# Kernel optimization log

Hardware: AMD Instinct MI355X
Metric: run time of the kernel (lower is better)

The kernel has to match this reference:

```python
import jax, jax.numpy as jnp
import numpy as np

B, S, H = 1, 2048, 2048
NH, KVH, D = 32, 8, 64
G = NH // KVH  # num_key_value_groups = 4


def setup_inputs() -> dict:
    key = jax.random.key(0)
    k1, k2, k3 = jax.random.split(key, 3)
    x = jax.random.normal(k1, (B, S, H), dtype=jnp.float32)
    w_qkv = jax.random.normal(k2, ((NH + 2 * KVH) * D, H), dtype=jnp.float32) * 0.02
    w_o = jax.random.normal(k3, (H, NH * D), dtype=jnp.float32) * 0.02
    return {"x": x, "w_qkv": w_qkv, "w_o": w_o}


def _rope_cos_sin(seqlen, dim, dtype):
    inv_freq = 1.0 / (10000.0 ** (jnp.arange(0, dim, 2, dtype=jnp.float32) / dim))
    t = jnp.arange(seqlen, dtype=jnp.float32)
    freqs = jnp.outer(t, inv_freq)  # [S, D/2]
    return jnp.cos(freqs).astype(dtype), jnp.sin(freqs).astype(dtype)


def _apply_rope(x, cos, sin):
    # x: [B,S,h,D]; non-interleaved half rotation (flash-attn RotaryEmbedding)
    d2 = x.shape[-1] // 2
    x1, x2 = x[..., :d2], x[..., d2:]
    c = cos[None, :, None, :]
    s = sin[None, :, None, :]
    return jnp.concatenate([x1 * c - x2 * s, x2 * c + x1 * s], axis=-1)


def reference(x, w_qkv, w_o):
    b, s, _ = x.shape
    qkv = x @ w_qkv.T  # fused QKV proj: [B,S,(NH+2*KVH)*D]
    q, kv = jnp.split(qkv, [NH * D], axis=-1)
    q = q.reshape(b, s, NH, D)
    kv = kv.reshape(b, s, 2, KVH, D)
    cos, sin = _rope_cos_sin(s, D, x.dtype)
    q = _apply_rope(q, cos, sin)
    k = _apply_rope(kv[:, :, 0], cos, sin)
    v = kv[:, :, 1]
    # GQA: group q heads per kv head instead of repeat_interleave (same math)
    qg = q.reshape(b, s, KVH, G, D)
    scale = 1.0 / np.sqrt(D).astype(np.float32)
    scores = jnp.einsum('bskgd,btkd->bkgst', qg, k) * scale  # [B,KVH,G,S,S]
    causal = jnp.tril(jnp.ones((s, s), dtype=bool))
    scores = jnp.where(causal[None, None, None], scores, jnp.asarray(-jnp.inf, scores.dtype))
    p = jax.nn.softmax(scores, axis=-1)
    out = jnp.einsum('bkgst,btkd->bskgd', p, v).reshape(b, s, NH * D)
    return out @ w_o.T
```

## Files before the change

kernel.cpp:

```cpp
#include <hip/hip_runtime.h>


typedef __bf16 bf16_t;
typedef __attribute__((ext_vector_type(8))) __bf16 bf16x8;
typedef __attribute__((ext_vector_type(4))) __bf16 bf16x4;
typedef __attribute__((ext_vector_type(4))) float f32x4;

#define S_LEN 2048
#define H_DIM 2048
#define NHEAD 32
#define KVH 8
#define HD 64
#define QKV_N 3072

#define ENT_STRIDE 8320

__global__ void cast3_kernel(const float* __restrict__ x, const float* __restrict__ wq,
                             const float* __restrict__ wo, bf16_t* __restrict__ xb,
                             bf16_t* __restrict__ wqb, bf16_t* __restrict__ wob) {
  int i = blockIdx.x * blockDim.x + threadIdx.x;
  const int n1 = S_LEN * H_DIM / 4, n2 = QKV_N * H_DIM / 4, n3 = H_DIM * H_DIM / 4;
  const float* src; bf16_t* dst; int j;
  if (i < n1)           { src = x;  dst = xb;  j = i; }
  else if (i < n1 + n2) { src = wq; dst = wqb; j = i - n1; }
  else if (i < n1 + n2 + n3) { src = wo; dst = wob; j = i - n1 - n2; }
  else return;
  float4 v = ((const float4*)src)[j];
  bf16x4 o;
  o.x = (bf16_t)v.x; o.y = (bf16_t)v.y; o.z = (bf16_t)v.z; o.w = (bf16_t)v.w;
  ((bf16x4*)dst)[j] = o;
}

__device__ __forceinline__ void async_copy16(bf16_t* lds_base, const bf16_t* g) {
  __builtin_amdgcn_global_load_lds(
      (const __attribute__((address_space(1))) unsigned int*)g,
      (__attribute__((address_space(3))) unsigned int*)lds_base, 16, 0, 0);
}

#define GBM 128
#define GBN 128

template <int EPI>
__global__ __launch_bounds__(512, 4) void gemm_sk(const bf16_t* __restrict__ A,
                                                  const bf16_t* __restrict__ B,
                                                  float* __restrict__ C,
                                                  bf16_t* __restrict__ qb,
                                                  bf16_t* __restrict__ ktp,
                                                  bf16_t* __restrict__ vt2,
                                                  int M, int N, int K) {
  __shared__ __align__(16) bf16_t As[2][GBM * 64];
  __shared__ __align__(16) bf16_t Bs[2][GBM * 64];

  const int tid  = threadIdx.x;
  const int lane = tid & 63;
  const int w    = tid >> 6;
  const int wq   = w & 3;
  const int gw   = w >> 2;
  const int wm   = (wq >> 1) * 64;
  const int wn   = (wq & 1) * 64;
  const int c    = lane & 15;
  const int quad = lane >> 4;
  const int m0   = blockIdx.y * GBM;
  const int n0   = blockIdx.x * GBN;

  f32x4 acc[4][4] = {};

  const bf16_t* Ab = A + (size_t)m0 * K;
  const bf16_t* Bb = B + (size_t)n0 * K;

  int srow[2], skc[2], sb[2];
#pragma unroll
  for (int i = 0; i < 2; ++i) {
    int p = i * 512 + tid;
    srow[i] = p >> 3;
    skc[i]  = (p & 7) ^ (srow[i] & 7);
    sb[i]   = (i * 512 + w * 64) * 8;
  }

  auto stage = [&](int buf, int k0) {
#pragma unroll
    for (int i = 0; i < 2; ++i) {
      async_copy16(&As[buf][sb[i]], Ab + (size_t)srow[i] * K + k0 + skc[i] * 8);
      async_copy16(&Bs[buf][sb[i]], Bb + (size_t)srow[i] * K + k0 + skc[i] * 8);
    }
  };

  auto compute = [&](int buf) {
    bf16x8 af[4], bfr[4];
#pragma unroll
    for (int mt = 0; mt < 4; ++mt) {
      int row = wm + mt * 16 + c;
      af[mt] = *(const bf16x8*)&As[buf][(row * 8 + ((gw * 4 + quad) ^ (row & 7))) * 8];
    }
#pragma unroll
    for (int nt = 0; nt < 4; ++nt) {
      int rowb = wn + nt * 16 + c;
      bfr[nt] = *(const bf16x8*)&Bs[buf][(rowb * 8 + ((gw * 4 + quad) ^ (rowb & 7))) * 8];
    }
#pragma unroll
    for (int mt = 0; mt < 4; ++mt)
#pragma unroll
      for (int nt = 0; nt < 4; ++nt)
        acc[mt][nt] = __builtin_amdgcn_mfma_f32_16x16x32_bf16(af[mt], bfr[nt], acc[mt][nt], 0, 0, 0);
  };

  const int NI = K >> 6;
  stage(0, 0);
  int buf = 0;
  for (int it = 0; it < NI; ++it) {
    asm volatile("s_waitcnt vmcnt(0)" ::: "memory");
    __builtin_amdgcn_s_barrier();
    if (it + 1 < NI) stage(buf ^ 1, (it + 1) << 6);
    compute(buf);
    buf ^= 1;
  }

  __syncthreads();
  float* xch = (float*)&As[0][0];
  if (gw == 1) {
#pragma unroll
    for (int t16 = 0; t16 < 16; ++t16)
      *(f32x4*)&xch[wq * 4096 + (t16 * 64 + lane) * 4] = acc[t16 >> 2][t16 & 3];
  }
  __syncthreads();
  if (gw == 0) {
#pragma unroll
    for (int t16 = 0; t16 < 16; ++t16) {
      f32x4 o = *(const f32x4*)&xch[wq * 4096 + (t16 * 64 + lane) * 4];
      acc[t16 >> 2][t16 & 3] += o;
    }

    if (EPI == 0) {
#pragma unroll
      for (int mt = 0; mt < 4; ++mt)
#pragma unroll
        for (int nt = 0; nt < 4; ++nt)
#pragma unroll
          for (int reg = 0; reg < 4; ++reg) {
            int row = m0 + wm + mt * 16 + quad * 4 + reg;
            int col = n0 + wn + nt * 16 + c;
            C[(size_t)row * N + col] = acc[mt][nt][reg];
          }
    } else {
      const int colb = n0 + wn;
      if (colb < NHEAD * HD) {
        const int h = colb >> 6;
#pragma unroll
        for (int nt = 0; nt < 2; ++nt) {
          const int i = nt * 16 + c;
          const float invf = __expf(-(float)i * (9.210340371976184f / 32.0f));
#pragma unroll
          for (int mt = 0; mt < 4; ++mt)
#pragma unroll
            for (int reg = 0; reg < 4; ++reg) {
              const int s = m0 + wm + mt * 16 + quad * 4 + reg;
              float sn, cs;
              __sincosf((float)s * invf, &sn, &cs);
              const float x1 = acc[mt][nt][reg], x2 = acc[mt][nt + 2][reg];
              bf16_t* q = qb + (size_t)s * H_DIM + h * HD;
              q[i]      = (bf16_t)((x1 * cs - x2 * sn) * 0.125f);
              q[i + 32] = (bf16_t)((x2 * cs + x1 * sn) * 0.125f);
            }
        }
      } else if (colb < NHEAD * HD + KVH * HD) {
        const int kh = (colb - NHEAD * HD) >> 6;
#pragma unroll
        for (int nt = 0; nt < 2; ++nt) {
          const int i = nt * 16 + c;
          const float invf = __expf(-(float)i * (9.210340371976184f / 32.0f));
#pragma unroll
          for (int mt = 0; mt < 4; ++mt)
#pragma unroll
            for (int reg = 0; reg < 4; ++reg) {
              const int s = m0 + wm + mt * 16 + quad * 4 + reg;
              float sn, cs;
              __sincosf((float)s * invf, &sn, &cs);
              const float x1 = acc[mt][nt][reg], x2 = acc[mt][nt + 2][reg];
              bf16_t* kd = ktp + ((size_t)kh * S_LEN + s) * HD;
              kd[i]      = (bf16_t)(x1 * cs - x2 * sn);
              kd[i + 32] = (bf16_t)(x2 * cs + x1 * sn);
            }
        }
      } else {
        const int kh = (colb - NHEAD * HD - KVH * HD) >> 6;
#pragma unroll
        for (int nt = 0; nt < 4; ++nt) {
          const int d = nt * 16 + c;
#pragma unroll
          for (int mt = 0; mt < 4; ++mt) {
            const int sr = m0 + wm + mt * 16 + quad * 4;
            bf16x4 pv;
#pragma unroll
            for (int reg = 0; reg < 4; ++reg) pv[reg] = (bf16_t)acc[mt][nt][reg];
            *(bf16x4*)&vt2[((size_t)kh * HD + d) * S_LEN + sr] = pv;
          }
        }
      }
    }
  }
}

#define PSTR 72

__global__ __launch_bounds__(256) void flash_split(const bf16_t* __restrict__ qb,
                                                   const bf16_t* __restrict__ kt,
                                                   const bf16_t* __restrict__ vt2,
                                                   float* __restrict__ pbuf,
                                                   bf16_t* __restrict__ attn) {
  __shared__ __align__(16) bf16_t Ks[2][64 * 64];
  __shared__ __align__(16) bf16_t Vs[2][64 * 64];
  __shared__ __align__(16) bf16_t Ps[4][32 * PSTR];

  const int tid  = threadIdx.x;
  const int lane = tid & 63;
  const int w    = tid >> 6;
  const int e    = (int)gridDim.x - 1 - (int)blockIdx.x;
  const int kh   = e / 160;
  const int i    = e - kh * 160;

  int qt, t_begin, t_end;
  {
    int T;
    if (i < 16)      { qt = i;                T = (qt >> 1) + 1; t_begin = 0;                 t_end = T; }
    else if (i < 48) { int r = i - 16; qt = 16 + (r >> 1); int ck = r & 1;
                       T = (qt >> 1) + 1; t_begin = (ck * T) >> 1;      t_end = ((ck + 1) * T) >> 1; }
    else if (i < 96) { int r = i - 48; qt = 32 + r / 3;    int ck = r % 3;
                       T = (qt >> 1) + 1; t_begin = (ck * T) / 3;       t_end = ((ck + 1) * T) / 3; }
    else             { int r = i - 96; qt = 48 + (r >> 2); int ck = r & 3;
                       T = (qt >> 1) + 1; t_begin = (ck * T) >> 2;      t_end = ((ck + 1) * T) >> 2; }
  }
  const int T     = (qt >> 1) + 1;
  const int s0    = qt * 32;
  const int h     = kh * 4 + w;
  const int c     = lane & 15;
  const int quad  = lane >> 4;

  bf16x8 qf[2][2];
#pragma unroll
  for (int rf = 0; rf < 2; ++rf)
#pragma unroll
    for (int ks = 0; ks < 2; ++ks)
      qf[rf][ks] = *(const bf16x8*)(qb + (size_t)(s0 + rf * 16 + c) * H_DIM + h * HD + ks * 32 + quad * 8);

  f32x4 acc[2][4] = {};
  float lsum[2] = {0.f, 0.f};

  const bf16_t* kbase = kt + (size_t)kh * S_LEN * HD;
  const bf16_t* vbase = vt2 + (size_t)kh * HD * S_LEN;

  int srow[2], skc[2], sbase[2];
#pragma unroll
  for (int i2 = 0; i2 < 2; ++i2) {
    int chunkbase = i2 * 256 + w * 64;
    int p = chunkbase + lane;
    sbase[i2] = chunkbase * 8;
    srow[i2]  = p >> 3;
    skc[i2]   = (p & 7) ^ (srow[i2] & 7);
  }

  auto stage = [&](int buf, int tile) {
    const int t0 = tile * 64;
#pragma unroll
    for (int i2 = 0; i2 < 2; ++i2) {
      async_copy16(&Ks[buf][sbase[i2]], kbase + (size_t)(t0 + srow[i2]) * HD + skc[i2] * 8);
      async_copy16(&Vs[buf][sbase[i2]], vbase + (size_t)srow[i2] * S_LEN + t0 + skc[i2] * 8);
    }
  };

  stage(0, t_begin);
  int buf = 0;
  for (int tile = t_begin; tile < t_end; ++tile) {
    const int t0 = tile * 64;
    asm volatile("s_waitcnt vmcnt(0)" ::: "memory");
    __builtin_amdgcn_s_barrier();
    if (tile + 1 < t_end) stage(buf ^ 1, tile + 1);

    const bool masked = (tile == T - 1);
    int nact = 4;
    if (masked) { nact = ((s0 + 31 - t0) >> 4) + 1; if (nact > 4) nact = 4; }
    const int nkh = (nact + 1) >> 1;

#pragma unroll
    for (int rf = 0; rf < 2; ++rf) {
      for (int kt2 = 0; kt2 < nact; ++kt2) {
        f32x4 st = {};
        __builtin_amdgcn_s_setprio(1);
#pragma unroll
        for (int ks = 0; ks < 2; ++ks) {
          bf16x8 kf = *(const bf16x8*)&Ks[buf][((kt2 * 16 + c) * 8 + ((ks * 4 + quad) ^ (c & 7))) * 8];
          st = __builtin_amdgcn_mfma_f32_16x16x32_bf16(kf, qf[rf][ks], st, 0, 0, 0);
        }
        __builtin_amdgcn_s_setprio(0);
        const int row = s0 + rf * 16 + c;
        bf16x4 pk;
#pragma unroll
        for (int reg = 0; reg < 4; ++reg) {
          const int key = t0 + kt2 * 16 + quad * 4 + reg;
          float p = __expf(st[reg] - 8.0f);
          if (masked && key > row) p = 0.f;
          pk[reg] = (bf16_t)p;
          lsum[rf] += p;
        }
        *(bf16x4*)&Ps[w][(rf * 16 + c) * PSTR + kt2 * 16 + quad * 4] = pk;
      }
      for (int kt2 = nact; kt2 < 2 * nkh; ++kt2) {
        bf16x4 z = {};
        *(bf16x4*)&Ps[w][(rf * 16 + c) * PSTR + kt2 * 16 + quad * 4] = z;
      }
    }

    for (int kh2 = 0; kh2 < nkh; ++kh2) {
      bf16x8 vf[4];
#pragma unroll
      for (int dt = 0; dt < 4; ++dt)
        vf[dt] = *(const bf16x8*)&Vs[buf][((dt * 16 + c) * 8 + ((kh2 * 4 + quad) ^ (c & 7))) * 8];
      __builtin_amdgcn_s_setprio(1);
#pragma unroll
      for (int rf = 0; rf < 2; ++rf) {
        bf16x8 pa = *(const bf16x8*)&Ps[w][(rf * 16 + c) * PSTR + kh2 * 32 + quad * 8];
#pragma unroll
        for (int dt = 0; dt < 4; ++dt)
          acc[rf][dt] = __builtin_amdgcn_mfma_f32_16x16x32_bf16(pa, vf[dt], acc[rf][dt], 0, 0, 0);
      }
      __builtin_amdgcn_s_setprio(0);
    }
    buf ^= 1;
  }

#pragma unroll
  for (int rf = 0; rf < 2; ++rf) {
    lsum[rf] += __shfl_xor(lsum[rf], 16);
    lsum[rf] += __shfl_xor(lsum[rf], 32);
  }

  if (i < 16) {
    float* lbuf = (float*)&Ps[w][0];
#pragma unroll
    for (int rf = 0; rf < 2; ++rf) lbuf[rf * 16 + c] = lsum[rf];
    asm volatile("s_waitcnt lgkmcnt(0)" ::: "memory");
#pragma unroll
    for (int rf = 0; rf < 2; ++rf)
#pragma unroll
      for (int reg = 0; reg < 4; ++reg) {
        const float inv = 1.0f / lbuf[rf * 16 + quad * 4 + reg];
        const int row = s0 + rf * 16 + quad * 4 + reg;
#pragma unroll
        for (int dt = 0; dt < 4; ++dt)
          attn[(size_t)row * H_DIM + h * HD + dt * 16 + c] = (bf16_t)(acc[rf][dt][reg] * inv);
      }
  } else {
    float* ent = pbuf + (size_t)e * ENT_STRIDE;
#pragma unroll
    for (int rf = 0; rf < 2; ++rf) {
#pragma unroll
      for (int dt = 0; dt < 4; ++dt)
#pragma unroll
        for (int reg = 0; reg < 4; ++reg)
          ent[w * 2048 + (rf * 16 + quad * 4 + reg) * 64 + dt * 16 + c] = acc[rf][dt][reg];
      ent[8192 + w * 32 + rf * 16 + c] = lsum[rf];
    }
  }
}

__global__ __launch_bounds__(256) void flash_reduce(const float* __restrict__ pbuf,
                                                    bf16_t* __restrict__ attn) {
  const int kh = blockIdx.x / 48;
  const int qt = 16 + (blockIdx.x % 48);
  const int b  = qt >> 4;
  int base;
  if (b == 1)      base = kh * 160 + 16 + (qt - 16) * 2;
  else if (b == 2) base = kh * 160 + 48 + (qt - 32) * 3;
  else             base = kh * 160 + 96 + (qt - 48) * 4;
  const int nch = b + 1;

  const int t   = threadIdx.x;
  const int h2  = t >> 6;
  const int row = (t >> 1) & 31;
  const int dh  = t & 1;

  f32x4 o[8] = {};
  float l = 0.f;
  for (int ci = 0; ci < nch; ++ci) {
    const float* ent = pbuf + (size_t)(base + ci) * ENT_STRIDE;
    const float* p = ent + h2 * 2048 + row * 64 + dh * 32;
#pragma unroll
    for (int j = 0; j < 8; ++j) {
      f32x4 v = ((const f32x4*)p)[j];
      o[j][0] += v[0]; o[j][1] += v[1]; o[j][2] += v[2]; o[j][3] += v[3];
    }
    l += ent[8192 + h2 * 32 + row];
  }
  const float inv = 1.0f / l;
  bf16_t* dst = attn + (size_t)(qt * 32 + row) * H_DIM + (kh * 4 + h2) * 64 + dh * 32;
#pragma unroll
  for (int j = 0; j < 8; ++j) {
    bf16x4 ov;
    ov[0] = (bf16_t)(o[j][0] * inv); ov[1] = (bf16_t)(o[j][1] * inv);
    ov[2] = (bf16_t)(o[j][2] * inv); ov[3] = (bf16_t)(o[j][3] * inv);
    *(bf16x4*)(dst + j * 4) = ov;
  }
}

extern "C" void kernel_launch(void* const* d_in, const int* in_sizes, int n_in,
                              void* d_out, int out_size, void* d_ws, size_t ws_size,
                              hipStream_t stream) {
  const float* x     = (const float*)d_in[0];
  const float* w_qkv = (const float*)d_in[1];
  const float* w_o   = (const float*)d_in[2];
  float* out = (float*)d_out;

  char* ws = (char*)d_ws;
  const size_t OVERLAY = (size_t)1280 * ENT_STRIDE * 4;
  bf16_t* x_bf    = (bf16_t*)ws;
  bf16_t* wqkv_bf = (bf16_t*)(ws + (size_t)S_LEN * H_DIM * 2);
  float*  pbuf    = (float*)ws;
  size_t off = OVERLAY;
  bf16_t* wo_bf   = (bf16_t*)(ws + off); off += (size_t)H_DIM * H_DIM * 2;
  bf16_t* q_bf    = (bf16_t*)(ws + off); off += (size_t)S_LEN * H_DIM * 2;
  bf16_t* k_t     = (bf16_t*)(ws + off); off += (size_t)KVH * S_LEN * HD * 2;
  bf16_t* v_t2    = (bf16_t*)(ws + off); off += (size_t)KVH * S_LEN * HD * 2;
  bf16_t* attn    = (bf16_t*)(ws + off); off += (size_t)S_LEN * H_DIM * 2;

  const int ntot = (S_LEN * H_DIM + QKV_N * H_DIM + H_DIM * H_DIM) / 4;
  cast3_kernel<<<(ntot + 255) / 256, 256, 0, stream>>>(x, w_qkv, w_o, x_bf, wqkv_bf, wo_bf);

  gemm_sk<1><<<dim3(QKV_N / GBN, S_LEN / GBM), 512, 0, stream>>>(
      x_bf, wqkv_bf, nullptr, q_bf, k_t, v_t2, S_LEN, QKV_N, H_DIM);

  flash_split<<<1280, 256, 0, stream>>>(q_bf, k_t, v_t2, pbuf, attn);
  flash_reduce<<<384, 256, 0, stream>>>(pbuf, attn);

  gemm_sk<0><<<dim3(H_DIM / GBN, S_LEN / GBM), 512, 0, stream>>>(
      attn, wo_bf, out, nullptr, nullptr, nullptr, S_LEN, H_DIM, H_DIM);
}
```

Measured before the change: 223.0 us.

## Pass P between MFMAs via ds_bpermute instead of LDS staging buffer

Drops the per-wave shared-memory P buffer. The score tile is now rearranged into the PV MFMA operand layout with cross-lane ds_bpermute shuffles held in registers. The masked-tile work skipping (nact/nkh) is removed, so the diagonal tile always computes all four key subtiles, and launch bounds now request 5 blocks per CU. The lower LDS use may allow higher occupancy, but each step now runs more bpermute instructions and wasted masked MFMAs, and register pressure rises.

```diff
diff --git a/kernel.cpp b/kernel.cpp
--- a/kernel.cpp
+++ b/kernel.cpp
@@ -5,6 +5,8 @@
 typedef __attribute__((ext_vector_type(8))) __bf16 bf16x8;
 typedef __attribute__((ext_vector_type(4))) __bf16 bf16x4;
 typedef __attribute__((ext_vector_type(4))) float f32x4;
+typedef __attribute__((ext_vector_type(2))) unsigned int u32x2;
+typedef __attribute__((ext_vector_type(4))) unsigned int u32x4;
 
 #define S_LEN 2048
 #define H_DIM 2048
@@ -200,16 +202,13 @@
   }
 }
 
-#define PSTR 72
-
-__global__ __launch_bounds__(256) void flash_split(const bf16_t* __restrict__ qb,
-                                                   const bf16_t* __restrict__ kt,
-                                                   const bf16_t* __restrict__ vt2,
-                                                   float* __restrict__ pbuf,
-                                                   bf16_t* __restrict__ attn) {
+__global__ __launch_bounds__(256, 5) void flash_split(const bf16_t* __restrict__ qb,
+                                                      const bf16_t* __restrict__ kt,
+                                                      const bf16_t* __restrict__ vt2,
+                                                      float* __restrict__ pbuf,
+                                                      bf16_t* __restrict__ attn) {
   __shared__ __align__(16) bf16_t Ks[2][64 * 64];
   __shared__ __align__(16) bf16_t Vs[2][64 * 64];
-  __shared__ __align__(16) bf16_t Ps[4][32 * PSTR];
 
   const int tid  = threadIdx.x;
   const int lane = tid & 63;
@@ -235,6 +234,10 @@
   const int c     = lane & 15;
   const int quad  = lane >> 4;
 
+  const int idx0 = (c + (quad & 1) * 32) * 4;
+  const int idx1 = idx0 + 64;
+  const bool hiY = quad >= 2;
+
   bf16x8 qf[2][2];
 #pragma unroll
   for (int rf = 0; rf < 2; ++rf)
@@ -276,53 +279,66 @@
     if (tile + 1 < t_end) stage(buf ^ 1, tile + 1);
 
     const bool masked = (tile == T - 1);
-    int nact = 4;
-    if (masked) { nact = ((s0 + 31 - t0) >> 4) + 1; if (nact > 4) nact = 4; }
-    const int nkh = (nact + 1) >> 1;
-
-#pragma unroll
-    for (int rf = 0; rf < 2; ++rf) {
-      for (int kt2 = 0; kt2 < nact; ++kt2) {
-        f32x4 st = {};
-        __builtin_amdgcn_s_setprio(1);
-#pragma unroll
-        for (int ks = 0; ks < 2; ++ks) {
-          bf16x8 kf = *(const bf16x8*)&Ks[buf][((kt2 * 16 + c) * 8 + ((ks * 4 + quad) ^ (c & 7))) * 8];
-          st = __builtin_amdgcn_mfma_f32_16x16x32_bf16(kf, qf[rf][ks], st, 0, 0, 0);
+
+#pragma unroll
+    for (int kh2 = 0; kh2 < 2; ++kh2) {
+      unsigned pw[2][2][2];
+#pragma unroll
+      for (int kt2l = 0; kt2l < 2; ++kt2l) {
+        const int kt2 = kh2 * 2 + kt2l;
+        bf16x8 kf0 = *(const bf16x8*)&Ks[buf][((kt2 * 16 + c) * 8 + ((quad) ^ (c & 7))) * 8];
+        bf16x8 kf1 = *(const bf16x8*)&Ks[buf][((kt2 * 16 + c) * 8 + ((4 + quad) ^ (c & 7))) * 8];
+#pragma unroll
+        for (int rf = 0; rf < 2; ++rf) {
+          f32x4 st = {};
+          __builtin_amdgcn_s_setprio(1);
+          st = __builtin_amdgcn_mfma_f32_16x16x32_bf16(kf0, qf[rf][0], st, 0, 0, 0);
+          st = __builtin_amdgcn_mfma_f32_16x16x32_bf16(kf1, qf[rf][1], st, 0, 0, 0);
+          __builtin_amdgcn_s_setprio(0);
+          const int row = s0 + rf * 16 + c;
+          bf16x4 pk;
+#pragma unroll
+          for (int reg = 0; reg < 4; ++reg) {
+            const int key = t0 + kt2 * 16 + quad * 4 + reg;
+            float p = __expf(st[reg] - 8.0f);
+            if (masked && key > row) p = 0.f;
+            pk[reg] = (bf16_t)p;
+            lsum[rf] += p;
+          }
+          u32x2 pv2 = __builtin_bit_cast(u32x2, pk);
+          pw[rf][kt2l][0] = pv2.x;
+          pw[rf][kt2l][1] = pv2.y;
         }
-        __builtin_amdgcn_s_setprio(0);
-        const int row = s0 + rf * 16 + c;
-        bf16x4 pk;
-#pragma unroll
-        for (int reg = 0; reg < 4; ++reg) {
-          const int key = t0 + kt2 * 16 + quad * 4 + reg;
-          float p = __expf(st[reg] - 8.0f);
-          if (masked && key > row) p = 0.f;
-          pk[reg] = (bf16_t)p;
-          lsum[rf] += p;
-        }
-        *(bf16x4*)&Ps[w][(rf * 16 + c) * PSTR + kt2 * 16 + quad * 4] = pk;
       }
-      for (int kt2 = nact; kt2 < 2 * nkh; ++kt2) {
-        bf16x4 z = {};
-        *(bf16x4*)&Ps[w][(rf * 16 + c) * PSTR + kt2 * 16 + quad * 4] = z;
-      }
-    }
-
-    for (int kh2 = 0; kh2 < nkh; ++kh2) {
+
       bf16x8 vf[4];
 #pragma unroll
       for (int dt = 0; dt < 4; ++dt)
         vf[dt] = *(const bf16x8*)&Vs[buf][((dt * 16 + c) * 8 + ((kh2 * 4 + quad) ^ (c & 7))) * 8];
-      __builtin_amdgcn_s_setprio(1);
+
 #pragma unroll
       for (int rf = 0; rf < 2; ++rf) {
-        bf16x8 pa = *(const bf16x8*)&Ps[w][(rf * 16 + c) * PSTR + kh2 * 32 + quad * 8];
+        int lo, hi;
+        u32x4 fwv;
+        lo = __builtin_amdgcn_ds_bpermute(idx0, (int)pw[rf][0][0]);
+        hi = __builtin_amdgcn_ds_bpermute(idx0, (int)pw[rf][1][0]);
+        fwv.x = hiY ? (unsigned)hi : (unsigned)lo;
+        lo = __builtin_amdgcn_ds_bpermute(idx0, (int)pw[rf][0][1]);
+        hi = __builtin_amdgcn_ds_bpermute(idx0, (int)pw[rf][1][1]);
+        fwv.y = hiY ? (unsigned)hi : (unsigned)lo;
+        lo = __builtin_amdgcn_ds_bpermute(idx1, (int)pw[rf][0][0]);
+        hi = __builtin_amdgcn_ds_bpermute(idx1, (int)pw[rf][1][0]);
+        fwv.z = hiY ? (unsigned)hi : (unsigned)lo;
+        lo = __builtin_amdgcn_ds_bpermute(idx1, (int)pw[rf][0][1]);
+        hi = __builtin_amdgcn_ds_bpermute(idx1, (int)pw[rf][1][1]);
+        fwv.w = hiY ? (unsigned)hi : (unsigned)lo;
+        bf16x8 pa = __builtin_bit_cast(bf16x8, fwv);
+        __builtin_amdgcn_s_setprio(1);
 #pragma unroll
         for (int dt = 0; dt < 4; ++dt)
           acc[rf][dt] = __builtin_amdgcn_mfma_f32_16x16x32_bf16(pa, vf[dt], acc[rf][dt], 0, 0, 0);
+        __builtin_amdgcn_s_setprio(0);
       }
-      __builtin_amdgcn_s_setprio(0);
     }
     buf ^= 1;
   }
@@ -333,8 +349,9 @@
     lsum[rf] += __shfl_xor(lsum[rf], 32);
   }
 
+  __syncthreads();
   if (i < 16) {
-    float* lbuf = (float*)&Ps[w][0];
+    float* lbuf = (float*)&Ks[0][0] + w * 32;
 #pragma unroll
     for (int rf = 0; rf < 2; ++rf) lbuf[rf * 16 + c] = lsum[rf];
     asm volatile("s_waitcnt lgkmcnt(0)" ::: "memory");
```

Result: slower. 238.5 us (+7.0%).
